# Kernel tuning notes

Measured on AMD Instinct MI355X. Metric: run time of the kernel, lower is better.

Reference implementation:

```python
import jax, jax.numpy as jnp
import numpy as np

N = 100000
E = 3200000
IN_C = 128
HID = 16
OUT_C = 16
EA = 16


def setup_inputs() -> dict:
    key = jax.random.key(0)
    ks = jax.random.split(key, 8)
    x = jax.random.normal(ks[0], (N, IN_C), dtype=jnp.float32)
    edge_index = jax.random.randint(ks[1], (2, E), 0, N, dtype=jnp.int32)
    edge_attr = jax.random.normal(ks[2], (E, EA), dtype=jnp.float32)
    We = jax.random.normal(ks[3], (EA, HID), dtype=jnp.float32) * (1.0 / np.sqrt(EA))
    be = jnp.zeros((HID,), dtype=jnp.float32)
    W1 = jax.random.normal(ks[4], (IN_C, HID), dtype=jnp.float32) * (1.0 / np.sqrt(IN_C))
    b1 = jnp.zeros((HID,), dtype=jnp.float32)
    W2 = jax.random.normal(ks[5], (HID, OUT_C), dtype=jnp.float32) * (1.0 / np.sqrt(HID))
    b2 = jnp.zeros((OUT_C,), dtype=jnp.float32)
    return {"x": x, "edge_index": edge_index, "edge_attr": edge_attr,
            "We": We, "be": be, "W1": W1, "b1": b1, "W2": W2, "b2": b2}


def _gcn_conv(h, src, dst, ew, dinv_src, dinv_dst, dinv_sq, W, b):
    # h: [N, Cin] -> transform first (PyG order), then normalized gather-scatter.
    h = h @ W                                   # [N, C], C == HID == OUT_C == 16
    norm = dinv_src * ew * dinv_dst             # [E, 16] per-edge per-channel norm
    msg = norm * h[src]                          # gather + fuse edge weight
    agg = jax.ops.segment_sum(msg, dst, num_segments=N)  # scatter-add
    agg = agg + dinv_sq * h                      # self-loop (weight 1) contribution
    return agg + b


def reference(x, edge_index, edge_attr, We, be, W1, b1, W2, b2):
    src, dst = edge_index[0], edge_index[1]
    ew = edge_attr @ We + be                     # [E, 16] edge weights (per channel)
    # symmetric degree normalization with self loops (weight 1), per channel
    deg = jax.ops.segment_sum(ew, dst, num_segments=N) + 1.0  # [N, 16]
    dinv = jnp.where(deg > 0, jax.lax.rsqrt(jnp.abs(deg) + 1e-12), 0.0)
    dinv_src = dinv[src]
    dinv_dst = dinv[dst]
    dinv_sq = dinv * dinv
    h = jax.nn.relu(_gcn_conv(x, src, dst, ew, dinv_src, dinv_dst, dinv_sq, W1, b1))
    # dropout is identity in eval mode
    out = _gcn_conv(h, src, dst, ew, dinv_src, dinv_dst, dinv_sq, W2, b2)
    return out
```

## Files before the change

kernel.cpp:

```cpp
#include <hip/hip_runtime.h>

static constexpr int N_NODES = 100000;
static constexpr int N_EDGES = 3200000;
static constexpr int NC16    = N_NODES * 16;
static constexpr int RB      = 128;
static constexpr int NB      = (N_NODES + RB - 1) / RB;
static constexpr int CAP     = 4800;
static constexpr int NPB     = 512;
static constexpr int EPB     = (N_EDGES + NPB - 1) / NPB;

__device__ __forceinline__ float4 v4fma(float s, float4 w, float4 acc) {
    acc.x = fmaf(s, w.x, acc.x);
    acc.y = fmaf(s, w.y, acc.y);
    acc.z = fmaf(s, w.z, acc.z);
    acc.w = fmaf(s, w.w, acc.w);
    return acc;
}

template<int KK>
__device__ __forceinline__ float4 qbcast(float4 a) {
    constexpr int ctrl = KK * 0x55;
    float4 r;
    r.x = __int_as_float(__builtin_amdgcn_mov_dpp(__float_as_int(a.x), ctrl, 0xF, 0xF, true));
    r.y = __int_as_float(__builtin_amdgcn_mov_dpp(__float_as_int(a.y), ctrl, 0xF, 0xF, true));
    r.z = __int_as_float(__builtin_amdgcn_mov_dpp(__float_as_int(a.z), ctrl, 0xF, 0xF, true));
    r.w = __int_as_float(__builtin_amdgcn_mov_dpp(__float_as_int(a.w), ctrl, 0xF, 0xF, true));
    return r;
}

template<int KK>
__device__ __forceinline__ float4 ewstep(float4 a, const float4* wc, float4 ew) {
    float4 v = qbcast<KK>(a);
    ew = v4fma(v.x, wc[4*KK + 0], ew);
    ew = v4fma(v.y, wc[4*KK + 1], ew);
    ew = v4fma(v.z, wc[4*KK + 2], ew);
    ew = v4fma(v.w, wc[4*KK + 3], ew);
    return ew;
}

__device__ __forceinline__ void accum4(double* __restrict__ accS, int dl, int c4,
                                       double v0, double v1, double v2, double v3) {
    double* row = accS + dl * 16;
    const int pb = (c4 * 4 + dl) & 15;
    atomicAdd(row + ((pb + 0) & 15), v0);
    atomicAdd(row + ((pb + 1) & 15), v1);
    atomicAdd(row + ((pb + 2) & 15), v2);
    atomicAdd(row + ((pb + 3) & 15), v3);
}

__global__ __launch_bounds__(256)
void k_zero(int* g) {
    int t = blockIdx.x * 256 + threadIdx.x;
    if (t < NB) g[t] = 0;
}

__global__ __launch_bounds__(1024)
void k_part(const int* __restrict__ srcI, const int* __restrict__ dstI,
            int* __restrict__ gcount, int2* __restrict__ meta)
{
    __shared__ int hist[NB];
    const int tid  = threadIdx.x;
    const int e0   = blockIdx.x * EPB;
    const int ecnt = min(EPB, N_EDGES - e0);
    for (int t = tid; t < NB; t += 1024) hist[t] = 0;
    __syncthreads();
    for (int i = tid; i < ecnt; i += 1024) {
        int d = dstI[e0 + i];
        atomicAdd(&hist[d >> 7], 1);
    }
    __syncthreads();
    for (int t = tid; t < NB; t += 1024) {
        int h = hist[t];
        hist[t] = (h > 0) ? atomicAdd(&gcount[t], h) : 0;
    }
    __syncthreads();
    for (int i = tid; i < ecnt; i += 1024) {
        int e = e0 + i;
        int d = dstI[e];
        int s = srcI[e];
        int b = d >> 7;
        int pos = atomicAdd(&hist[b], 1);
        if (pos < CAP)
            meta[b * CAP + pos] = make_int2(e, (s << 7) | (d & 127));
    }
}

template<int MODE>
__global__ __launch_bounds__(512)
void k_bucket(const float* __restrict__ ea, const int2* __restrict__ meta,
              const int* __restrict__ gcount, const float* __restrict__ We,
              const float* __restrict__ be, const float* __restrict__ p,
              float* __restrict__ outv)
{
    __shared__ double accS[RB * 16];
    const int tid = threadIdx.x;
    const int b   = blockIdx.x;
    for (int t = tid; t < RB * 16; t += 512) accS[t] = 0.0;

    const int c4 = tid & 3;
    float4 wc[16];
    const float4* We4 = (const float4*)We;
#pragma unroll
    for (int k = 0; k < 16; ++k) wc[k] = We4[k * 4 + c4];
    const float4 bev = ((const float4*)be)[c4];
    const int cnt = min(gcount[b], CAP);
    const int2* ml = meta + b * CAP;
    const float4* ea4 = (const float4*)ea;
    const float4* p4  = (const float4*)p;
    __syncthreads();

#pragma unroll 2
    for (int i = tid >> 2; i < cnt; i += 128) {
        int2 m = ml[i];
        float4 a = ea4[m.x * 4 + c4];
        float4 pv;
        if (MODE == 1) pv = p4[((unsigned)m.y >> 7) * 4 + c4];
        const int dl = m.y & 127;
        float4 ew = bev;
        ew = ewstep<0>(a, wc, ew);
        ew = ewstep<1>(a, wc, ew);
        ew = ewstep<2>(a, wc, ew);
        ew = ewstep<3>(a, wc, ew);
        if (MODE == 1) {
            accum4(accS, dl, c4,
                   (double)(ew.x * pv.x), (double)(ew.y * pv.y),
                   (double)(ew.z * pv.z), (double)(ew.w * pv.w));
        } else {
            accum4(accS, dl, c4, (double)ew.x, (double)ew.y, (double)ew.z, (double)ew.w);
        }
    }
    __syncthreads();

    for (int t = tid; t < RB * 4; t += 512) {
        int nl = t >> 2;
        int ng = b * RB + nl;
        if (ng < N_NODES) {
            const double* s = accS + nl * 16;
            const int pb = ((t & 3) * 4 + nl) & 15;
            float4 o;
            if (MODE == 0) {
                float d0 = (float)s[(pb + 0) & 15] + 1.0f; o.x = (d0 > 0.f) ? rsqrtf(d0 + 1e-12f) : 0.f;
                float d1 = (float)s[(pb + 1) & 15] + 1.0f; o.y = (d1 > 0.f) ? rsqrtf(d1 + 1e-12f) : 0.f;
                float d2 = (float)s[(pb + 2) & 15] + 1.0f; o.z = (d2 > 0.f) ? rsqrtf(d2 + 1e-12f) : 0.f;
                float d3 = (float)s[(pb + 3) & 15] + 1.0f; o.w = (d3 > 0.f) ? rsqrtf(d3 + 1e-12f) : 0.f;
            } else {
                o.x = (float)s[(pb + 0) & 15];
                o.y = (float)s[(pb + 1) & 15];
                o.z = (float)s[(pb + 2) & 15];
                o.w = (float)s[(pb + 3) & 15];
            }
            ((float4*)outv)[ng * 4 + (t & 3)] = o;
        }
    }
}

__global__ __launch_bounds__(256)
void k_xw1(const float* __restrict__ x, const float* __restrict__ W1,
           const float* __restrict__ dinv, float* __restrict__ p)
{
    __shared__ float4 w1s[512];
    const int t = threadIdx.x;
    const float4* W14 = (const float4*)W1;
    w1s[t]       = W14[t];
    w1s[t + 256] = W14[t + 256];
    __syncthreads();

    const int c4 = t & 3;
    const int nl = t >> 2;
    const int nb = blockIdx.x * 256;
    int node[4];
    float4 acc[4];
#pragma unroll
    for (int i = 0; i < 4; ++i) {
        node[i] = nb + i * 64 + nl;
        acc[i]  = make_float4(0.f, 0.f, 0.f, 0.f);
    }
    const float4* x4 = (const float4*)x;

    for (int k4 = 0; k4 < 32; ++k4) {
        float4 wv0 = w1s[(k4 * 4 + 0) * 4 + c4];
        float4 wv1 = w1s[(k4 * 4 + 1) * 4 + c4];
        float4 wv2 = w1s[(k4 * 4 + 2) * 4 + c4];
        float4 wv3 = w1s[(k4 * 4 + 3) * 4 + c4];
#pragma unroll
        for (int i = 0; i < 4; ++i) {
            int nn = node[i] < N_NODES ? node[i] : (N_NODES - 1);
            float4 xv = x4[nn * 32 + k4];
            acc[i] = v4fma(xv.x, wv0, acc[i]);
            acc[i] = v4fma(xv.y, wv1, acc[i]);
            acc[i] = v4fma(xv.z, wv2, acc[i]);
            acc[i] = v4fma(xv.w, wv3, acc[i]);
        }
    }
    const float4* dinv4 = (const float4*)dinv;
    float4* pp = (float4*)p;
#pragma unroll
    for (int i = 0; i < 4; ++i) {
        if (node[i] < N_NODES) {
            float4 dv = dinv4[node[i] * 4 + c4];
            float4 o;
            o.x = dv.x * acc[i].x; o.y = dv.y * acc[i].y;
            o.z = dv.z * acc[i].z; o.w = dv.w * acc[i].w;
            pp[node[i] * 4 + c4] = o;
        }
    }
}

__global__ __launch_bounds__(256)
void k_mid(const float* __restrict__ accA, const float* __restrict__ dinv,
           const float* __restrict__ W2, const float* __restrict__ b1,
           float* __restrict__ p)
{
    const int tid = blockIdx.x * 256 + threadIdx.x;
    const int q   = tid >> 2;
    if (q >= N_NODES) return;
    const int c4 = threadIdx.x & 3;

    float4 wc[16];
    const float4* W24 = (const float4*)W2;
#pragma unroll
    for (int k = 0; k < 16; ++k) wc[k] = W24[k * 4 + c4];
    const float4 b1v = ((const float4*)b1)[c4];

    const float4 av = ((const float4*)accA)[q * 4 + c4];
    const float4 pv = ((const float4*)p)[q * 4 + c4];
    const float4 dv = ((const float4*)dinv)[q * 4 + c4];

    float4 h1;
    h1.x = fmaxf(fmaf(dv.x, av.x + pv.x, b1v.x), 0.f);
    h1.y = fmaxf(fmaf(dv.y, av.y + pv.y, b1v.y), 0.f);
    h1.z = fmaxf(fmaf(dv.z, av.z + pv.z, b1v.z), 0.f);
    h1.w = fmaxf(fmaf(dv.w, av.w + pv.w, b1v.w), 0.f);

    float4 h2 = make_float4(0.f, 0.f, 0.f, 0.f);
    h2 = ewstep<0>(h1, wc, h2);
    h2 = ewstep<1>(h1, wc, h2);
    h2 = ewstep<2>(h1, wc, h2);
    h2 = ewstep<3>(h1, wc, h2);

    float4 o;
    o.x = dv.x * h2.x; o.y = dv.y * h2.y;
    o.z = dv.z * h2.z; o.w = dv.w * h2.w;
    ((float4*)p)[q * 4 + c4] = o;
}

__global__ __launch_bounds__(256)
void k_out(const float* __restrict__ accB, const float* __restrict__ dinv,
           const float* __restrict__ p, const float* __restrict__ b2,
           float* __restrict__ out)
{
    const int tid = blockIdx.x * 256 + threadIdx.x;
    const int q   = tid >> 2;
    if (q >= N_NODES) return;
    const int c4 = threadIdx.x & 3;
    const float4 b2v = ((const float4*)b2)[c4];
    const float4 av = ((const float4*)accB)[q * 4 + c4];
    const float4 pv = ((const float4*)p)[q * 4 + c4];
    const float4 dv = ((const float4*)dinv)[q * 4 + c4];
    float4 o;
    o.x = fmaf(dv.x, av.x + pv.x, b2v.x);
    o.y = fmaf(dv.y, av.y + pv.y, b2v.y);
    o.z = fmaf(dv.z, av.z + pv.z, b2v.z);
    o.w = fmaf(dv.w, av.w + pv.w, b2v.w);
    ((float4*)out)[q * 4 + c4] = o;
}

extern "C" void kernel_launch(void* const* d_in, const int* in_sizes, int n_in,
                              void* d_out, int out_size, void* d_ws, size_t ws_size,
                              hipStream_t stream)
{
    const float* x   = (const float*)d_in[0];
    const int*   ei  = (const int*)d_in[1];
    const float* ea  = (const float*)d_in[2];
    const float* We  = (const float*)d_in[3];
    const float* be  = (const float*)d_in[4];
    const float* W1  = (const float*)d_in[5];
    const float* b1  = (const float*)d_in[6];
    const float* W2  = (const float*)d_in[7];
    const float* b2  = (const float*)d_in[8];
    float* out = (float*)d_out;

    const int* srcI = ei;
    const int* dstI = ei + N_EDGES;

    float* dinv = (float*)d_ws;
    float* p    = dinv + NC16;
    float* accA = p + NC16;
    float* accB = accA + NC16;
    int2*  meta = (int2*)(accB + NC16);
    int*   gcount = (int*)(meta + (size_t)NB * CAP);

    const dim3 blk(256);
    hipLaunchKernelGGL(k_zero, dim3((NB + 255) / 256), blk, 0, stream, gcount);
    hipLaunchKernelGGL(k_part, dim3(NPB), dim3(1024), 0, stream,
                       srcI, dstI, gcount, meta);
    hipLaunchKernelGGL((k_bucket<0>), dim3(NB), dim3(512), 0, stream,
                       ea, meta, gcount, We, be, (const float*)nullptr, dinv);
    hipLaunchKernelGGL(k_xw1, dim3((N_NODES + 255) / 256), blk, 0, stream,
                       x, W1, dinv, p);
    hipLaunchKernelGGL((k_bucket<1>), dim3(NB), dim3(512), 0, stream,
                       ea, meta, gcount, We, be, p, accA);
    hipLaunchKernelGGL(k_mid, dim3((N_NODES * 4 + 255) / 256), blk, 0, stream,
                       accA, dinv, W2, b1, p);
    hipLaunchKernelGGL((k_bucket<1>), dim3(NB), dim3(512), 0, stream,
                       ea, meta, gcount, We, be, p, accB);
    hipLaunchKernelGGL(k_out, dim3((N_NODES * 4 + 255) / 256), blk, 0, stream,
                       accB, dinv, p, b2, out);
}
```

Before: 682.2 us.

## Precompute edge weights once during partition and stream bucket-sorted records

```diff
diff --git a/kernel.cpp b/kernel.cpp
--- a/kernel.cpp
+++ b/kernel.cpp
@@ -7,7 +7,7 @@
 static constexpr int NB      = (N_NODES + RB - 1) / RB;
 static constexpr int CAP     = 4800;
 static constexpr int NPB     = 512;
-static constexpr int EPB     = (N_EDGES + NPB - 1) / NPB;
+static constexpr int EPB     = N_EDGES / NPB;
 
 __device__ __forceinline__ float4 v4fma(float s, float4 w, float4 acc) {
     acc.x = fmaf(s, w.x, acc.x);
@@ -54,48 +54,61 @@
     if (t < NB) g[t] = 0;
 }
 
-__global__ __launch_bounds__(1024)
-void k_part(const int* __restrict__ srcI, const int* __restrict__ dstI,
-            int* __restrict__ gcount, int2* __restrict__ meta)
+__global__ __launch_bounds__(512)
+void k_part_ew(const int* __restrict__ srcI, const int* __restrict__ dstI,
+               const float* __restrict__ ea, const float* __restrict__ We,
+               const float* __restrict__ be,
+               int* __restrict__ gcount,
+               float4* __restrict__ ewRec4, int* __restrict__ metaRec)
 {
     __shared__ int hist[NB];
-    const int tid  = threadIdx.x;
-    const int e0   = blockIdx.x * EPB;
-    const int ecnt = min(EPB, N_EDGES - e0);
-    for (int t = tid; t < NB; t += 1024) hist[t] = 0;
-    __syncthreads();
-    for (int i = tid; i < ecnt; i += 1024) {
-        int d = dstI[e0 + i];
-        atomicAdd(&hist[d >> 7], 1);
-    }
-    __syncthreads();
-    for (int t = tid; t < NB; t += 1024) {
+    __shared__ int lpref[NB];
+    __shared__ int gbase[NB];
+    __shared__ int tsum[512];
+    __shared__ int eidS[EPB];
+    __shared__ unsigned short bS[EPB];
+    const int tid = threadIdx.x;
+    const int e0  = blockIdx.x * EPB;
+
+    for (int t = tid; t < NB; t += 512) hist[t] = 0;
+    __syncthreads();
+    for (int i = tid; i < EPB; i += 512)
+        atomicAdd(&hist[dstI[e0 + i] >> 7], 1);
+    __syncthreads();
+
+    int a0 = (2 * tid     < NB) ? hist[2 * tid]     : 0;
+    int a1 = (2 * tid + 1 < NB) ? hist[2 * tid + 1] : 0;
+    tsum[tid] = a0 + a1;
+    __syncthreads();
+    for (int off = 1; off < 512; off <<= 1) {
+        int v = tsum[tid];
+        if (tid >= off) v += tsum[tid - off];
+        __syncthreads();
+        tsum[tid] = v;
+        __syncthreads();
+    }
+    {
+        int ex = tid ? tsum[tid - 1] : 0;
+        if (2 * tid     < NB) lpref[2 * tid]     = ex;
+        if (2 * tid + 1 < NB) lpref[2 * tid + 1] = ex + a0;
+    }
+    __syncthreads();
+
+    for (int t = tid; t < NB; t += 512) {
         int h = hist[t];
-        hist[t] = (h > 0) ? atomicAdd(&gcount[t], h) : 0;
-    }
-    __syncthreads();
-    for (int i = tid; i < ecnt; i += 1024) {
+        gbase[t] = (h > 0) ? atomicAdd(&gcount[t], h) : 0;
+        hist[t] = 0;
+    }
+    __syncthreads();
+
+    for (int i = tid; i < EPB; i += 512) {
         int e = e0 + i;
-        int d = dstI[e];
-        int s = srcI[e];
-        int b = d >> 7;
-        int pos = atomicAdd(&hist[b], 1);
-        if (pos < CAP)
-            meta[b * CAP + pos] = make_int2(e, (s << 7) | (d & 127));
-    }
-}
-
-template<int MODE>
-__global__ __launch_bounds__(512)
-void k_bucket(const float* __restrict__ ea, const int2* __restrict__ meta,
-              const int* __restrict__ gcount, const float* __restrict__ We,
-              const float* __restrict__ be, const float* __restrict__ p,
-              float* __restrict__ outv)
-{
-    __shared__ double accS[RB * 16];
-    const int tid = threadIdx.x;
-    const int b   = blockIdx.x;
-    for (int t = tid; t < RB * 16; t += 512) accS[t] = 0.0;
+        int b = dstI[e] >> 7;
+        int slot = lpref[b] + atomicAdd(&hist[b], 1);
+        eidS[slot] = e;
+        bS[slot] = (unsigned short)b;
+    }
+    __syncthreads();
 
     const int c4 = tid & 3;
     float4 wc[16];
@@ -103,31 +116,57 @@
 #pragma unroll
     for (int k = 0; k < 16; ++k) wc[k] = We4[k * 4 + c4];
     const float4 bev = ((const float4*)be)[c4];
-    const int cnt = min(gcount[b], CAP);
-    const int2* ml = meta + b * CAP;
     const float4* ea4 = (const float4*)ea;
-    const float4* p4  = (const float4*)p;
-    __syncthreads();
-
-#pragma unroll 2
-    for (int i = tid >> 2; i < cnt; i += 128) {
-        int2 m = ml[i];
-        float4 a = ea4[m.x * 4 + c4];
-        float4 pv;
-        if (MODE == 1) pv = p4[((unsigned)m.y >> 7) * 4 + c4];
-        const int dl = m.y & 127;
+
+#pragma unroll 4
+    for (int j = tid >> 2; j < EPB; j += 128) {
+        int e = eidS[j];
+        int b = bS[j];
+        int idx = gbase[b] + (j - lpref[b]);
+        float4 a = ea4[e * 4 + c4];
         float4 ew = bev;
         ew = ewstep<0>(a, wc, ew);
         ew = ewstep<1>(a, wc, ew);
         ew = ewstep<2>(a, wc, ew);
         ew = ewstep<3>(a, wc, ew);
+        if (idx < CAP) {
+            int r = b * CAP + idx;
+            ewRec4[r * 4 + c4] = ew;
+            if (c4 == 0) {
+                int s = srcI[e];
+                int d = dstI[e];
+                metaRec[r] = (s << 7) | (d & 127);
+            }
+        }
+    }
+}
+
+template<int MODE>
+__global__ __launch_bounds__(512)
+void k_stream(const float4* __restrict__ ewRec4, const int* __restrict__ metaRec,
+              const int* __restrict__ gcount, const float* __restrict__ p,
+              float* __restrict__ outv)
+{
+    __shared__ double accS[RB * 16];
+    const int tid = threadIdx.x;
+    const int b   = blockIdx.x;
+    for (int t = tid; t < RB * 16; t += 512) accS[t] = 0.0;
+    const int c4  = tid & 3;
+    const int cnt = min(gcount[b], CAP);
+    const int base = b * CAP;
+    const float4* p4 = (const float4*)p;
+    __syncthreads();
+
+#pragma unroll 4
+    for (int i = tid >> 2; i < cnt; i += 128) {
+        float4 ew = ewRec4[(base + i) * 4 + c4];
+        int m = metaRec[base + i];
         if (MODE == 1) {
-            accum4(accS, dl, c4,
-                   (double)(ew.x * pv.x), (double)(ew.y * pv.y),
-                   (double)(ew.z * pv.z), (double)(ew.w * pv.w));
-        } else {
-            accum4(accS, dl, c4, (double)ew.x, (double)ew.y, (double)ew.z, (double)ew.w);
-        }
+            float4 pv = p4[((unsigned)m >> 7) * 4 + c4];
+            ew.x *= pv.x; ew.y *= pv.y; ew.z *= pv.z; ew.w *= pv.w;
+        }
+        accum4(accS, m & 127, c4,
+               (double)ew.x, (double)ew.y, (double)ew.z, (double)ew.w);
     }
     __syncthreads();
 
@@ -154,6 +193,106 @@
     }
 }
 
+__global__ __launch_bounds__(1024)
+void k_part(const int* __restrict__ srcI, const int* __restrict__ dstI,
+            int* __restrict__ gcount, int2* __restrict__ meta)
+{
+    __shared__ int hist[NB];
+    const int tid  = threadIdx.x;
+    const int e0   = blockIdx.x * EPB;
+    const int ecnt = min(EPB, N_EDGES - e0);
+    for (int t = tid; t < NB; t += 1024) hist[t] = 0;
+    __syncthreads();
+    for (int i = tid; i < ecnt; i += 1024) {
+        int d = dstI[e0 + i];
+        atomicAdd(&hist[d >> 7], 1);
+    }
+    __syncthreads();
+    for (int t = tid; t < NB; t += 1024) {
+        int h = hist[t];
+        hist[t] = (h > 0) ? atomicAdd(&gcount[t], h) : 0;
+    }
+    __syncthreads();
+    for (int i = tid; i < ecnt; i += 1024) {
+        int e = e0 + i;
+        int d = dstI[e];
+        int s = srcI[e];
+        int b = d >> 7;
+        int pos = atomicAdd(&hist[b], 1);
+        if (pos < CAP)
+            meta[b * CAP + pos] = make_int2(e, (s << 7) | (d & 127));
+    }
+}
+
+template<int MODE>
+__global__ __launch_bounds__(512)
+void k_bucket(const float* __restrict__ ea, const int2* __restrict__ meta,
+              const int* __restrict__ gcount, const float* __restrict__ We,
+              const float* __restrict__ be, const float* __restrict__ p,
+              float* __restrict__ outv)
+{
+    __shared__ double accS[RB * 16];
+    const int tid = threadIdx.x;
+    const int b   = blockIdx.x;
+    for (int t = tid; t < RB * 16; t += 512) accS[t] = 0.0;
+
+    const int c4 = tid & 3;
+    float4 wc[16];
+    const float4* We4 = (const float4*)We;
+#pragma unroll
+    for (int k = 0; k < 16; ++k) wc[k] = We4[k * 4 + c4];
+    const float4 bev = ((const float4*)be)[c4];
+    const int cnt = min(gcount[b], CAP);
+    const int2* ml = meta + b * CAP;
+    const float4* ea4 = (const float4*)ea;
+    const float4* p4  = (const float4*)p;
+    __syncthreads();
+
+#pragma unroll 2
+    for (int i = tid >> 2; i < cnt; i += 128) {
+        int2 m = ml[i];
+        float4 a = ea4[m.x * 4 + c4];
+        float4 pv;
+        if (MODE == 1) pv = p4[((unsigned)m.y >> 7) * 4 + c4];
+        const int dl = m.y & 127;
+        float4 ew = bev;
+        ew = ewstep<0>(a, wc, ew);
+        ew = ewstep<1>(a, wc, ew);
+        ew = ewstep<2>(a, wc, ew);
+        ew = ewstep<3>(a, wc, ew);
+        if (MODE == 1) {
+            accum4(accS, dl, c4,
+                   (double)(ew.x * pv.x), (double)(ew.y * pv.y),
+                   (double)(ew.z * pv.z), (double)(ew.w * pv.w));
+        } else {
+            accum4(accS, dl, c4, (double)ew.x, (double)ew.y, (double)ew.z, (double)ew.w);
+        }
+    }
+    __syncthreads();
+
+    for (int t = tid; t < RB * 4; t += 512) {
+        int nl = t >> 2;
+        int ng = b * RB + nl;
+        if (ng < N_NODES) {
+            const double* s = accS + nl * 16;
+            const int pb = ((t & 3) * 4 + nl) & 15;
+            float4 o;
+            if (MODE == 0) {
+                float d0 = (float)s[(pb + 0) & 15] + 1.0f; o.x = (d0 > 0.f) ? rsqrtf(d0 + 1e-12f) : 0.f;
+                float d1 = (float)s[(pb + 1) & 15] + 1.0f; o.y = (d1 > 0.f) ? rsqrtf(d1 + 1e-12f) : 0.f;
+                float d2 = (float)s[(pb + 2) & 15] + 1.0f; o.z = (d2 > 0.f) ? rsqrtf(d2 + 1e-12f) : 0.f;
+                float d3 = (float)s[(pb + 3) & 15] + 1.0f; o.w = (d3 > 0.f) ? rsqrtf(d3 + 1e-12f) : 0.f;
+            } else {
+                o.x = (float)s[(pb + 0) & 15];
+                o.y = (float)s[(pb + 1) & 15];
+                o.z = (float)s[(pb + 2) & 15];
+                o.w = (float)s[(pb + 3) & 15];
+            }
+            ((float4*)outv)[ng * 4 + (t & 3)] = o;
+        }
+    }
+}
+
 __global__ __launch_bounds__(256)
 void k_xw1(const float* __restrict__ x, const float* __restrict__ W1,
            const float* __restrict__ dinv, float* __restrict__ p)
@@ -287,23 +426,51 @@
     float* p    = dinv + NC16;
     float* accA = p + NC16;
     float* accB = accA + NC16;
-    int2*  meta = (int2*)(accB + NC16);
-    int*   gcount = (int*)(meta + (size_t)NB * CAP);
+
+    const size_t needA = (size_t)4 * NC16 * 4
+                       + (size_t)NB * CAP * (sizeof(float4) * 4 + sizeof(int))
+                       + (size_t)NB * sizeof(int) + 4096;
 
     const dim3 blk(256);
-    hipLaunchKernelGGL(k_zero, dim3((NB + 255) / 256), blk, 0, stream, gcount);
-    hipLaunchKernelGGL(k_part, dim3(NPB), dim3(1024), 0, stream,
-                       srcI, dstI, gcount, meta);
-    hipLaunchKernelGGL((k_bucket<0>), dim3(NB), dim3(512), 0, stream,
-                       ea, meta, gcount, We, be, (const float*)nullptr, dinv);
-    hipLaunchKernelGGL(k_xw1, dim3((N_NODES + 255) / 256), blk, 0, stream,
-                       x, W1, dinv, p);
-    hipLaunchKernelGGL((k_bucket<1>), dim3(NB), dim3(512), 0, stream,
-                       ea, meta, gcount, We, be, p, accA);
-    hipLaunchKernelGGL(k_mid, dim3((N_NODES * 4 + 255) / 256), blk, 0, stream,
-                       accA, dinv, W2, b1, p);
-    hipLaunchKernelGGL((k_bucket<1>), dim3(NB), dim3(512), 0, stream,
-                       ea, meta, gcount, We, be, p, accB);
-    hipLaunchKernelGGL(k_out, dim3((N_NODES * 4 + 255) / 256), blk, 0, stream,
-                       accB, dinv, p, b2, out);
-}
+
+    if (ws_size >= needA) {
+        float4* ewRec4 = (float4*)(accB + NC16);
+        int*    metaRec = (int*)(ewRec4 + (size_t)NB * CAP * 4);
+        int*    gcount  = metaRec + (size_t)NB * CAP;
+
+        hipLaunchKernelGGL(k_zero, dim3((NB + 255) / 256), blk, 0, stream, gcount);
+        hipLaunchKernelGGL(k_part_ew, dim3(NPB), dim3(512), 0, stream,
+                           srcI, dstI, ea, We, be, gcount, ewRec4, metaRec);
+        hipLaunchKernelGGL((k_stream<0>), dim3(NB), dim3(512), 0, stream,
+                           ewRec4, metaRec, gcount, (const float*)nullptr, dinv);
+        hipLaunchKernelGGL(k_xw1, dim3((N_NODES + 255) / 256), blk, 0, stream,
+                           x, W1, dinv, p);
+        hipLaunchKernelGGL((k_stream<1>), dim3(NB), dim3(512), 0, stream,
+                           ewRec4, metaRec, gcount, p, accA);
+        hipLaunchKernelGGL(k_mid, dim3((N_NODES * 4 + 255) / 256), blk, 0, stream,
+                           accA, dinv, W2, b1, p);
+        hipLaunchKernelGGL((k_stream<1>), dim3(NB), dim3(512), 0, stream,
+                           ewRec4, metaRec, gcount, p, accB);
+        hipLaunchKernelGGL(k_out, dim3((N_NODES * 4 + 255) / 256), blk, 0, stream,
+                           accB, dinv, p, b2, out);
+    } else {
+        int2* meta   = (int2*)(accB + NC16);
+        int*  gcount = (int*)(meta + (size_t)NB * CAP);
+
+        hipLaunchKernelGGL(k_zero, dim3((NB + 255) / 256), blk, 0, stream, gcount);
+        hipLaunchKernelGGL(k_part, dim3(NPB), dim3(1024), 0, stream,
+                           srcI, dstI, gcount, meta);
+        hipLaunchKernelGGL((k_bucket<0>), dim3(NB), dim3(512), 0, stream,
+                           ea, meta, gcount, We, be, (const float*)nullptr, dinv);
+        hipLaunchKernelGGL(k_xw1, dim3((N_NODES + 255) / 256), blk, 0, stream,
+                           x, W1, dinv, p);
+        hipLaunchKernelGGL((k_bucket<1>), dim3(NB), dim3(512), 0, stream,
+                           ea, meta, gcount, We, be, p, accA);
+        hipLaunchKernelGGL(k_mid, dim3((N_NODES * 4 + 255) / 256), blk, 0, stream,
+                           accA, dinv, W2, b1, p);
+        hipLaunchKernelGGL((k_bucket<1>), dim3(NB), dim3(512), 0, stream,
+                           ea, meta, gcount, We, be, p, accB);
+        hipLaunchKernelGGL(k_out, dim3((N_NODES * 4 + 255) / 256), blk, 0, stream,
+                           accB, dinv, p, b2, out);
+    }
+}
```

New measurement: 679.5 us. About the same (-0.4%).

## Fuse node-wise epilogues into bucket kernels and halve destination bucket size

Applied to the files above, without the earlier changes.

```diff
diff --git a/kernel.cpp b/kernel.cpp
--- a/kernel.cpp
+++ b/kernel.cpp
@@ -3,11 +3,11 @@
 static constexpr int N_NODES = 100000;
 static constexpr int N_EDGES = 3200000;
 static constexpr int NC16    = N_NODES * 16;
-static constexpr int RB      = 128;
+static constexpr int RB      = 64;
 static constexpr int NB      = (N_NODES + RB - 1) / RB;
-static constexpr int CAP     = 4800;
+static constexpr int CAP     = 2560;
 static constexpr int NPB     = 512;
-static constexpr int EPB     = (N_EDGES + NPB - 1) / NPB;
+static constexpr int EPB     = N_EDGES / NPB;
 
 __device__ __forceinline__ float4 v4fma(float s, float4 w, float4 acc) {
     acc.x = fmaf(s, w.x, acc.x);
@@ -59,14 +59,13 @@
             int* __restrict__ gcount, int2* __restrict__ meta)
 {
     __shared__ int hist[NB];
-    const int tid  = threadIdx.x;
-    const int e0   = blockIdx.x * EPB;
-    const int ecnt = min(EPB, N_EDGES - e0);
+    const int tid = threadIdx.x;
+    const int e0  = blockIdx.x * EPB;
     for (int t = tid; t < NB; t += 1024) hist[t] = 0;
     __syncthreads();
-    for (int i = tid; i < ecnt; i += 1024) {
+    for (int i = tid; i < EPB; i += 1024) {
         int d = dstI[e0 + i];
-        atomicAdd(&hist[d >> 7], 1);
+        atomicAdd(&hist[d >> 6], 1);
     }
     __syncthreads();
     for (int t = tid; t < NB; t += 1024) {
@@ -74,28 +73,30 @@
         hist[t] = (h > 0) ? atomicAdd(&gcount[t], h) : 0;
     }
     __syncthreads();
-    for (int i = tid; i < ecnt; i += 1024) {
+    for (int i = tid; i < EPB; i += 1024) {
         int e = e0 + i;
         int d = dstI[e];
         int s = srcI[e];
-        int b = d >> 7;
+        int b = d >> 6;
         int pos = atomicAdd(&hist[b], 1);
         if (pos < CAP)
-            meta[b * CAP + pos] = make_int2(e, (s << 7) | (d & 127));
-    }
-}
-
-template<int MODE>
+            meta[b * CAP + pos] = make_int2(e, (s << 6) | (d & 63));
+    }
+}
+
 __global__ __launch_bounds__(512)
-void k_bucket(const float* __restrict__ ea, const int2* __restrict__ meta,
-              const int* __restrict__ gcount, const float* __restrict__ We,
-              const float* __restrict__ be, const float* __restrict__ p,
-              float* __restrict__ outv)
+void k_deg(const float* __restrict__ ea, const int2* __restrict__ meta,
+           const int* __restrict__ gcount, const float* __restrict__ We,
+           const float* __restrict__ be,
+           const float* __restrict__ x, const float* __restrict__ W1,
+           float* __restrict__ dinv, float* __restrict__ pA)
 {
     __shared__ double accS[RB * 16];
+    __shared__ float4 w1s[512];
     const int tid = threadIdx.x;
     const int b   = blockIdx.x;
     for (int t = tid; t < RB * 16; t += 512) accS[t] = 0.0;
+    w1s[tid] = ((const float4*)W1)[tid];
 
     const int c4 = tid & 3;
     float4 wc[16];
@@ -106,163 +107,136 @@
     const int cnt = min(gcount[b], CAP);
     const int2* ml = meta + b * CAP;
     const float4* ea4 = (const float4*)ea;
-    const float4* p4  = (const float4*)p;
     __syncthreads();
 
 #pragma unroll 2
     for (int i = tid >> 2; i < cnt; i += 128) {
         int2 m = ml[i];
         float4 a = ea4[m.x * 4 + c4];
-        float4 pv;
-        if (MODE == 1) pv = p4[((unsigned)m.y >> 7) * 4 + c4];
-        const int dl = m.y & 127;
+        const int dl = m.y & 63;
         float4 ew = bev;
         ew = ewstep<0>(a, wc, ew);
         ew = ewstep<1>(a, wc, ew);
         ew = ewstep<2>(a, wc, ew);
         ew = ewstep<3>(a, wc, ew);
-        if (MODE == 1) {
-            accum4(accS, dl, c4,
-                   (double)(ew.x * pv.x), (double)(ew.y * pv.y),
-                   (double)(ew.z * pv.z), (double)(ew.w * pv.w));
-        } else {
-            accum4(accS, dl, c4, (double)ew.x, (double)ew.y, (double)ew.z, (double)ew.w);
-        }
-    }
-    __syncthreads();
-
-    for (int t = tid; t < RB * 4; t += 512) {
-        int nl = t >> 2;
-        int ng = b * RB + nl;
+        accum4(accS, dl, c4, (double)ew.x, (double)ew.y, (double)ew.z, (double)ew.w);
+    }
+    __syncthreads();
+
+    if (tid < RB * 4) {
+        const int nl = tid >> 2;
+        const int ng = b * RB + nl;
         if (ng < N_NODES) {
             const double* s = accS + nl * 16;
-            const int pb = ((t & 3) * 4 + nl) & 15;
+            const int pb = (c4 * 4 + nl) & 15;
+            float4 dv;
+            float d0 = (float)s[(pb + 0) & 15] + 1.0f; dv.x = (d0 > 0.f) ? rsqrtf(d0 + 1e-12f) : 0.f;
+            float d1 = (float)s[(pb + 1) & 15] + 1.0f; dv.y = (d1 > 0.f) ? rsqrtf(d1 + 1e-12f) : 0.f;
+            float d2 = (float)s[(pb + 2) & 15] + 1.0f; dv.z = (d2 > 0.f) ? rsqrtf(d2 + 1e-12f) : 0.f;
+            float d3 = (float)s[(pb + 3) & 15] + 1.0f; dv.w = (d3 > 0.f) ? rsqrtf(d3 + 1e-12f) : 0.f;
+            ((float4*)dinv)[ng * 4 + c4] = dv;
+
+            const float4* x4 = (const float4*)x;
+            float4 acc = make_float4(0.f, 0.f, 0.f, 0.f);
+            for (int k4 = 0; k4 < 32; ++k4) {
+                float4 xv = x4[ng * 32 + k4];
+                acc = v4fma(xv.x, w1s[(k4 * 4 + 0) * 4 + c4], acc);
+                acc = v4fma(xv.y, w1s[(k4 * 4 + 1) * 4 + c4], acc);
+                acc = v4fma(xv.z, w1s[(k4 * 4 + 2) * 4 + c4], acc);
+                acc = v4fma(xv.w, w1s[(k4 * 4 + 3) * 4 + c4], acc);
+            }
             float4 o;
-            if (MODE == 0) {
-                float d0 = (float)s[(pb + 0) & 15] + 1.0f; o.x = (d0 > 0.f) ? rsqrtf(d0 + 1e-12f) : 0.f;
-                float d1 = (float)s[(pb + 1) & 15] + 1.0f; o.y = (d1 > 0.f) ? rsqrtf(d1 + 1e-12f) : 0.f;
-                float d2 = (float)s[(pb + 2) & 15] + 1.0f; o.z = (d2 > 0.f) ? rsqrtf(d2 + 1e-12f) : 0.f;
-                float d3 = (float)s[(pb + 3) & 15] + 1.0f; o.w = (d3 > 0.f) ? rsqrtf(d3 + 1e-12f) : 0.f;
+            o.x = dv.x * acc.x; o.y = dv.y * acc.y;
+            o.z = dv.z * acc.z; o.w = dv.w * acc.w;
+            ((float4*)pA)[ng * 4 + c4] = o;
+        }
+    }
+}
+
+template<int FIN>
+__global__ __launch_bounds__(512)
+void k_gather(const float* __restrict__ ea, const int2* __restrict__ meta,
+              const int* __restrict__ gcount, const float* __restrict__ We,
+              const float* __restrict__ be, const float* __restrict__ dinv,
+              const float* __restrict__ pin, const float* __restrict__ Wb,
+              const float* __restrict__ b1, float* __restrict__ pout)
+{
+    __shared__ double accS[RB * 16];
+    const int tid = threadIdx.x;
+    const int b   = blockIdx.x;
+    for (int t = tid; t < RB * 16; t += 512) accS[t] = 0.0;
+
+    const int c4 = tid & 3;
+    float4 wc[16];
+    const float4* We4 = (const float4*)We;
+#pragma unroll
+    for (int k = 0; k < 16; ++k) wc[k] = We4[k * 4 + c4];
+    const float4 bev = ((const float4*)be)[c4];
+    const int cnt = min(gcount[b], CAP);
+    const int2* ml = meta + b * CAP;
+    const float4* ea4 = (const float4*)ea;
+    const float4* p4  = (const float4*)pin;
+    __syncthreads();
+
+#pragma unroll 2
+    for (int i = tid >> 2; i < cnt; i += 128) {
+        int2 m = ml[i];
+        float4 a = ea4[m.x * 4 + c4];
+        float4 pv = p4[((unsigned)m.y >> 6) * 4 + c4];
+        const int dl = m.y & 63;
+        float4 ew = bev;
+        ew = ewstep<0>(a, wc, ew);
+        ew = ewstep<1>(a, wc, ew);
+        ew = ewstep<2>(a, wc, ew);
+        ew = ewstep<3>(a, wc, ew);
+        accum4(accS, dl, c4,
+               (double)(ew.x * pv.x), (double)(ew.y * pv.y),
+               (double)(ew.z * pv.z), (double)(ew.w * pv.w));
+    }
+    __syncthreads();
+
+    if (tid < RB * 4) {
+        const int nl = tid >> 2;
+        const int ng = b * RB + nl;
+        if (ng < N_NODES) {
+            const double* s = accS + nl * 16;
+            const int pb = (c4 * 4 + nl) & 15;
+            float4 av;
+            av.x = (float)s[(pb + 0) & 15];
+            av.y = (float)s[(pb + 1) & 15];
+            av.z = (float)s[(pb + 2) & 15];
+            av.w = (float)s[(pb + 3) & 15];
+            const float4 pv = ((const float4*)pin)[ng * 4 + c4];
+            const float4 dv = ((const float4*)dinv)[ng * 4 + c4];
+            float4 o;
+            if (FIN == 0) {
+                const float4 b1v = ((const float4*)b1)[c4];
+                float4 h1;
+                h1.x = fmaxf(fmaf(dv.x, av.x + pv.x, b1v.x), 0.f);
+                h1.y = fmaxf(fmaf(dv.y, av.y + pv.y, b1v.y), 0.f);
+                h1.z = fmaxf(fmaf(dv.z, av.z + pv.z, b1v.z), 0.f);
+                h1.w = fmaxf(fmaf(dv.w, av.w + pv.w, b1v.w), 0.f);
+                float4 wc2[16];
+                const float4* W24 = (const float4*)Wb;
+#pragma unroll
+                for (int k = 0; k < 16; ++k) wc2[k] = W24[k * 4 + c4];
+                float4 h2 = make_float4(0.f, 0.f, 0.f, 0.f);
+                h2 = ewstep<0>(h1, wc2, h2);
+                h2 = ewstep<1>(h1, wc2, h2);
+                h2 = ewstep<2>(h1, wc2, h2);
+                h2 = ewstep<3>(h1, wc2, h2);
+                o.x = dv.x * h2.x; o.y = dv.y * h2.y;
+                o.z = dv.z * h2.z; o.w = dv.w * h2.w;
             } else {
-                o.x = (float)s[(pb + 0) & 15];
-                o.y = (float)s[(pb + 1) & 15];
-                o.z = (float)s[(pb + 2) & 15];
-                o.w = (float)s[(pb + 3) & 15];
+                const float4 b2v = ((const float4*)Wb)[c4];
+                o.x = fmaf(dv.x, av.x + pv.x, b2v.x);
+                o.y = fmaf(dv.y, av.y + pv.y, b2v.y);
+                o.z = fmaf(dv.z, av.z + pv.z, b2v.z);
+                o.w = fmaf(dv.w, av.w + pv.w, b2v.w);
             }
-            ((float4*)outv)[ng * 4 + (t & 3)] = o;
+            ((float4*)pout)[ng * 4 + c4] = o;
         }
     }
-}
-
-__global__ __launch_bounds__(256)
-void k_xw1(const float* __restrict__ x, const float* __restrict__ W1,
-           const float* __restrict__ dinv, float* __restrict__ p)
-{
-    __shared__ float4 w1s[512];
-    const int t = threadIdx.x;
-    const float4* W14 = (const float4*)W1;
-    w1s[t]       = W14[t];
-    w1s[t + 256] = W14[t + 256];
-    __syncthreads();
-
-    const int c4 = t & 3;
-    const int nl = t >> 2;
-    const int nb = blockIdx.x * 256;
-    int node[4];
-    float4 acc[4];
-#pragma unroll
-    for (int i = 0; i < 4; ++i) {
-        node[i] = nb + i * 64 + nl;
-        acc[i]  = make_float4(0.f, 0.f, 0.f, 0.f);
-    }
-    const float4* x4 = (const float4*)x;
-
-    for (int k4 = 0; k4 < 32; ++k4) {
-        float4 wv0 = w1s[(k4 * 4 + 0) * 4 + c4];
-        float4 wv1 = w1s[(k4 * 4 + 1) * 4 + c4];
-        float4 wv2 = w1s[(k4 * 4 + 2) * 4 + c4];
-        float4 wv3 = w1s[(k4 * 4 + 3) * 4 + c4];
-#pragma unroll
-        for (int i = 0; i < 4; ++i) {
-            int nn = node[i] < N_NODES ? node[i] : (N_NODES - 1);
-            float4 xv = x4[nn * 32 + k4];
-            acc[i] = v4fma(xv.x, wv0, acc[i]);
-            acc[i] = v4fma(xv.y, wv1, acc[i]);
-            acc[i] = v4fma(xv.z, wv2, acc[i]);
-            acc[i] = v4fma(xv.w, wv3, acc[i]);
-        }
-    }
-    const float4* dinv4 = (const float4*)dinv;
-    float4* pp = (float4*)p;
-#pragma unroll
-    for (int i = 0; i < 4; ++i) {
-        if (node[i] < N_NODES) {
-            float4 dv = dinv4[node[i] * 4 + c4];
-            float4 o;
-            o.x = dv.x * acc[i].x; o.y = dv.y * acc[i].y;
-            o.z = dv.z * acc[i].z; o.w = dv.w * acc[i].w;
-            pp[node[i] * 4 + c4] = o;
-        }
-    }
-}
-
-__global__ __launch_bounds__(256)
-void k_mid(const float* __restrict__ accA, const float* __restrict__ dinv,
-           const float* __restrict__ W2, const float* __restrict__ b1,
-           float* __restrict__ p)
-{
-    const int tid = blockIdx.x * 256 + threadIdx.x;
-    const int q   = tid >> 2;
-    if (q >= N_NODES) return;
-    const int c4 = threadIdx.x & 3;
-
-    float4 wc[16];
-    const float4* W24 = (const float4*)W2;
-#pragma unroll
-    for (int k = 0; k < 16; ++k) wc[k] = W24[k * 4 + c4];
-    const float4 b1v = ((const float4*)b1)[c4];
-
-    const float4 av = ((const float4*)accA)[q * 4 + c4];
-    const float4 pv = ((const float4*)p)[q * 4 + c4];
-    const float4 dv = ((const float4*)dinv)[q * 4 + c4];
-
-    float4 h1;
-    h1.x = fmaxf(fmaf(dv.x, av.x + pv.x, b1v.x), 0.f);
-    h1.y = fmaxf(fmaf(dv.y, av.y + pv.y, b1v.y), 0.f);
-    h1.z = fmaxf(fmaf(dv.z, av.z + pv.z, b1v.z), 0.f);
-    h1.w = fmaxf(fmaf(dv.w, av.w + pv.w, b1v.w), 0.f);
-
-    float4 h2 = make_float4(0.f, 0.f, 0.f, 0.f);
-    h2 = ewstep<0>(h1, wc, h2);
-    h2 = ewstep<1>(h1, wc, h2);
-    h2 = ewstep<2>(h1, wc, h2);
-    h2 = ewstep<3>(h1, wc, h2);
-
-    float4 o;
-    o.x = dv.x * h2.x; o.y = dv.y * h2.y;
-    o.z = dv.z * h2.z; o.w = dv.w * h2.w;
-    ((float4*)p)[q * 4 + c4] = o;
-}
-
-__global__ __launch_bounds__(256)
-void k_out(const float* __restrict__ accB, const float* __restrict__ dinv,
-           const float* __restrict__ p, const float* __restrict__ b2,
-           float* __restrict__ out)
-{
-    const int tid = blockIdx.x * 256 + threadIdx.x;
-    const int q   = tid >> 2;
-    if (q >= N_NODES) return;
-    const int c4 = threadIdx.x & 3;
-    const float4 b2v = ((const float4*)b2)[c4];
-    const float4 av = ((const float4*)accB)[q * 4 + c4];
-    const float4 pv = ((const float4*)p)[q * 4 + c4];
-    const float4 dv = ((const float4*)dinv)[q * 4 + c4];
-    float4 o;
-    o.x = fmaf(dv.x, av.x + pv.x, b2v.x);
-    o.y = fmaf(dv.y, av.y + pv.y, b2v.y);
-    o.z = fmaf(dv.z, av.z + pv.z, b2v.z);
-    o.w = fmaf(dv.w, av.w + pv.w, b2v.w);
-    ((float4*)out)[q * 4 + c4] = o;
 }
 
 extern "C" void kernel_launch(void* const* d_in, const int* in_sizes, int n_in,
@@ -284,26 +258,18 @@
     const int* dstI = ei + N_EDGES;
 
     float* dinv = (float*)d_ws;
-    float* p    = dinv + NC16;
-    float* accA = p + NC16;
-    float* accB = accA + NC16;
-    int2*  meta = (int2*)(accB + NC16);
+    float* pA   = dinv + NC16;
+    float* pB   = pA + NC16;
+    int2*  meta = (int2*)(pB + NC16);
     int*   gcount = (int*)(meta + (size_t)NB * CAP);
 
-    const dim3 blk(256);
-    hipLaunchKernelGGL(k_zero, dim3((NB + 255) / 256), blk, 0, stream, gcount);
+    hipLaunchKernelGGL(k_zero, dim3((NB + 255) / 256), dim3(256), 0, stream, gcount);
     hipLaunchKernelGGL(k_part, dim3(NPB), dim3(1024), 0, stream,
                        srcI, dstI, gcount, meta);
-    hipLaunchKernelGGL((k_bucket<0>), dim3(NB), dim3(512), 0, stream,
-                       ea, meta, gcount, We, be, (const float*)nullptr, dinv);
-    hipLaunchKernelGGL(k_xw1, dim3((N_NODES + 255) / 256), blk, 0, stream,
-                       x, W1, dinv, p);
-    hipLaunchKernelGGL((k_bucket<1>), dim3(NB), dim3(512), 0, stream,
-                       ea, meta, gcount, We, be, p, accA);
-    hipLaunchKernelGGL(k_mid, dim3((N_NODES * 4 + 255) / 256), blk, 0, stream,
-                       accA, dinv, W2, b1, p);
-    hipLaunchKernelGGL((k_bucket<1>), dim3(NB), dim3(512), 0, stream,
-                       ea, meta, gcount, We, be, p, accB);
-    hipLaunchKernelGGL(k_out, dim3((N_NODES * 4 + 255) / 256), blk, 0, stream,
-                       accB, dinv, p, b2, out);
-}
+    hipLaunchKernelGGL(k_deg, dim3(NB), dim3(512), 0, stream,
+                       ea, meta, gcount, We, be, x, W1, dinv, pA);
+    hipLaunchKernelGGL((k_gather<0>), dim3(NB), dim3(512), 0, stream,
+                       ea, meta, gcount, We, be, dinv, pA, W2, b1, pB);
+    hipLaunchKernelGGL((k_gather<1>), dim3(NB), dim3(512), 0, stream,
+                       ea, meta, gcount, We, be, dinv, pB, b2, (const float*)nullptr, out);
+}
```

Result: no change. 685.4 us (+0.5%).
